# Optimization experiments

Measured on AMD Instinct MI355X. Metric: run time of the kernel, lower is better.

Reference implementation:

```python
import jax, jax.numpy as jnp
import numpy as np

BINS = 64
EPS = 1e-8


def _compute_histogram(gray, bins=BINS):
    # gray: [B, H, W] -> normalized histogram [B, bins]
    B = gray.shape[0]
    flat = gray.reshape(B, -1)                      # [B, N]
    mn = flat.min(axis=1, keepdims=True)
    mx = flat.max(axis=1, keepdims=True)
    valid = mx > mn                                  # [B, 1]
    norm = (flat - mn) / jnp.where(valid, mx - mn, 1.0)
    idx = jnp.clip((norm * (bins - 1)).astype(jnp.int32), 0, bins - 1)  # [B, N]
    # per-image bincount via scatter-add
    hist = jax.vmap(lambda i: jnp.zeros(bins, dtype=flat.dtype).at[i].add(1.0))(idx)
    hist = hist / hist.sum(axis=1, keepdims=True)
    return jnp.where(valid, hist, jnp.full_like(hist, 1.0 / bins))


def reference(x, y, lambda_cc=10.0):
    # channel balance
    x_mean = jnp.mean(x, axis=(2, 3), keepdims=True)   # [B,3,1,1]
    y_mean = jnp.mean(y, axis=(2, 3), keepdims=True)
    x_bal = x_mean / (jnp.sum(x_mean, axis=1, keepdims=True) + EPS)
    y_bal = y_mean / (jnp.sum(y_mean, axis=1, keepdims=True) + EPS)
    color_balance_loss = jnp.mean(jnp.abs(x_bal - y_bal))

    # luminance
    x_gray = 0.299 * x[:, 0] + 0.587 * x[:, 1] + 0.114 * x[:, 2]  # [B,H,W]
    y_gray = 0.299 * y[:, 0] + 0.587 * y[:, 1] + 0.114 * y[:, 2]

    x_hist = _compute_histogram(x_gray)
    y_hist = _compute_histogram(y_gray)

    # F.kl_div(log(x_hist+eps), y_hist, reduction='batchmean')
    log_in = jnp.log(x_hist + EPS)
    ylogy = jnp.where(y_hist > 0, y_hist * jnp.log(jnp.where(y_hist > 0, y_hist, 1.0)), 0.0)
    kl = jnp.sum(ylogy - y_hist * log_in) / x.shape[0]

    return lambda_cc * (color_balance_loss + kl)


def setup_inputs() -> dict:
    key = jax.random.key(0)
    k1, k2 = jax.random.split(key)
    x = jax.random.uniform(k1, (16, 3, 512, 512), dtype=jnp.float32)
    y = jax.random.uniform(k2, (16, 3, 512, 512), dtype=jnp.float32)
    return {"x": x, "y": y}
```

## Files before the change

kernel.cpp:

```cpp
#include <hip/hip_runtime.h>

#define HW_N (512 * 512)
#define BINS 64
#define BPI 64
#define TPB 256

struct ImgStats {
    double sumx[3];
    double sumy[3];
    unsigned int minx, maxx, miny, maxy;
    unsigned int histx[BINS];
    unsigned int histy[BINS];
};

__device__ __forceinline__ unsigned int f2ord(float f) {
    unsigned int u = __float_as_uint(f);
    return (u & 0x80000000u) ? ~u : (u | 0x80000000u);
}
__device__ __forceinline__ float ord2f(unsigned int u) {
    u = (u & 0x80000000u) ? (u ^ 0x80000000u) : ~u;
    return __uint_as_float(u);
}

__device__ __forceinline__ float grayf(float r, float g, float b) {
    return 0.299f * r + 0.587f * g + 0.114f * b;
}

__device__ __forceinline__ double waveSumD(double v) {
#pragma unroll
    for (int o = 32; o > 0; o >>= 1) v += __shfl_down(v, o);
    return v;
}
__device__ __forceinline__ float waveMinF(float v) {
#pragma unroll
    for (int o = 32; o > 0; o >>= 1) v = fminf(v, __shfl_down(v, o));
    return v;
}
__device__ __forceinline__ float waveMaxF(float v) {
#pragma unroll
    for (int o = 32; o > 0; o >>= 1) v = fmaxf(v, __shfl_down(v, o));
    return v;
}

__global__ void k_init(ImgStats* st, int B) {
    const int nwords = B * (int)(sizeof(ImgStats) / 4);
    unsigned int* w = (unsigned int*)st;
    for (int i = threadIdx.x; i < nwords; i += blockDim.x) w[i] = 0u;
    __syncthreads();
    for (int i = threadIdx.x; i < B * 2; i += blockDim.x) {
        int b = i >> 1;
        if (i & 1) st[b].miny = 0xFFFFFFFFu;
        else       st[b].minx = 0xFFFFFFFFu;
    }
}

__global__ __launch_bounds__(TPB) void k_reduce_gray(const float* __restrict__ x,
                                                     const float* __restrict__ y,
                                                     ImgStats* __restrict__ st,
                                                     float4* __restrict__ gx,
                                                     float4* __restrict__ gy) {
    const int b   = blockIdx.x / BPI;
    const int sub = blockIdx.x % BPI;
    const int qPerBlock = (HW_N / 4) / BPI;
    const int q0 = sub * qPerBlock;
    const size_t base = (size_t)b * 3 * HW_N;
    const size_t gbase = (size_t)b * (HW_N / 4);

    const float4* xr = (const float4*)(x + base);
    const float4* xg = (const float4*)(x + base + HW_N);
    const float4* xb = (const float4*)(x + base + 2 * HW_N);
    const float4* yr = (const float4*)(y + base);
    const float4* yg = (const float4*)(y + base + HW_N);
    const float4* yb = (const float4*)(y + base + 2 * HW_N);

    float s0 = 0.f, s1 = 0.f, s2 = 0.f;
    float t0 = 0.f, t1 = 0.f, t2 = 0.f;
    float mnx = 3.4e38f, mxx = -3.4e38f;
    float mny = 3.4e38f, mxy = -3.4e38f;

    for (int i = threadIdx.x; i < qPerBlock; i += TPB) {
        const int q = q0 + i;
        float4 r = xr[q], g = xg[q], bl = xb[q];
        s0 += (r.x + r.y) + (r.z + r.w);
        s1 += (g.x + g.y) + (g.z + g.w);
        s2 += (bl.x + bl.y) + (bl.z + bl.w);
        {
            float4 gv = make_float4(grayf(r.x, g.x, bl.x), grayf(r.y, g.y, bl.y),
                                    grayf(r.z, g.z, bl.z), grayf(r.w, g.w, bl.w));
            gx[gbase + q] = gv;
            mnx = fminf(mnx, fminf(fminf(gv.x, gv.y), fminf(gv.z, gv.w)));
            mxx = fmaxf(mxx, fmaxf(fmaxf(gv.x, gv.y), fmaxf(gv.z, gv.w)));
        }
        r = yr[q]; g = yg[q]; bl = yb[q];
        t0 += (r.x + r.y) + (r.z + r.w);
        t1 += (g.x + g.y) + (g.z + g.w);
        t2 += (bl.x + bl.y) + (bl.z + bl.w);
        {
            float4 gv = make_float4(grayf(r.x, g.x, bl.x), grayf(r.y, g.y, bl.y),
                                    grayf(r.z, g.z, bl.z), grayf(r.w, g.w, bl.w));
            gy[gbase + q] = gv;
            mny = fminf(mny, fminf(fminf(gv.x, gv.y), fminf(gv.z, gv.w)));
            mxy = fmaxf(mxy, fmaxf(fmaxf(gv.x, gv.y), fmaxf(gv.z, gv.w)));
        }
    }

    const int wave = threadIdx.x >> 6;
    const int lane = threadIdx.x & 63;
    __shared__ double shs[6][TPB / 64];
    __shared__ float  shmn[2][TPB / 64];
    __shared__ float  shmx[2][TPB / 64];

    double d;
    d = waveSumD((double)s0); if (!lane) shs[0][wave] = d;
    d = waveSumD((double)s1); if (!lane) shs[1][wave] = d;
    d = waveSumD((double)s2); if (!lane) shs[2][wave] = d;
    d = waveSumD((double)t0); if (!lane) shs[3][wave] = d;
    d = waveSumD((double)t1); if (!lane) shs[4][wave] = d;
    d = waveSumD((double)t2); if (!lane) shs[5][wave] = d;
    float f;
    f = waveMinF(mnx); if (!lane) shmn[0][wave] = f;
    f = waveMinF(mny); if (!lane) shmn[1][wave] = f;
    f = waveMaxF(mxx); if (!lane) shmx[0][wave] = f;
    f = waveMaxF(mxy); if (!lane) shmx[1][wave] = f;
    __syncthreads();

    if (threadIdx.x == 0) {
        atomicAdd(&st[b].sumx[0], shs[0][0] + shs[0][1] + shs[0][2] + shs[0][3]);
        atomicAdd(&st[b].sumx[1], shs[1][0] + shs[1][1] + shs[1][2] + shs[1][3]);
        atomicAdd(&st[b].sumx[2], shs[2][0] + shs[2][1] + shs[2][2] + shs[2][3]);
        atomicAdd(&st[b].sumy[0], shs[3][0] + shs[3][1] + shs[3][2] + shs[3][3]);
        atomicAdd(&st[b].sumy[1], shs[4][0] + shs[4][1] + shs[4][2] + shs[4][3]);
        atomicAdd(&st[b].sumy[2], shs[5][0] + shs[5][1] + shs[5][2] + shs[5][3]);
        float a;
        a = fminf(fminf(shmn[0][0], shmn[0][1]), fminf(shmn[0][2], shmn[0][3]));
        atomicMin(&st[b].minx, f2ord(a));
        a = fminf(fminf(shmn[1][0], shmn[1][1]), fminf(shmn[1][2], shmn[1][3]));
        atomicMin(&st[b].miny, f2ord(a));
        a = fmaxf(fmaxf(shmx[0][0], shmx[0][1]), fmaxf(shmx[0][2], shmx[0][3]));
        atomicMax(&st[b].maxx, f2ord(a));
        a = fmaxf(fmaxf(shmx[1][0], shmx[1][1]), fmaxf(shmx[1][2], shmx[1][3]));
        atomicMax(&st[b].maxy, f2ord(a));
    }
}

__global__ __launch_bounds__(TPB) void k_hist_gray(const float4* __restrict__ gx,
                                                   const float4* __restrict__ gy,
                                                   ImgStats* __restrict__ st) {
    __shared__ unsigned int lh[16][BINS];
    for (int i = threadIdx.x; i < 16 * BINS; i += TPB) ((unsigned int*)lh)[i] = 0u;

    const int b   = blockIdx.x / BPI;
    const int sub = blockIdx.x % BPI;

    const float mnx = ord2f(st[b].minx), mxx = ord2f(st[b].maxx);
    const float mny = ord2f(st[b].miny), mxy = ord2f(st[b].maxy);
    const float rgx = (mxx > mnx) ? (mxx - mnx) : 1.0f;
    const float rgy = (mxy > mny) ? (mxy - mny) : 1.0f;
    __syncthreads();

    const int qPerBlock = (HW_N / 4) / BPI;
    const int q0 = sub * qPerBlock;
    const size_t gbase = (size_t)b * (HW_N / 4);

    const int wave = threadIdx.x >> 6;
    const int half = (threadIdx.x >> 5) & 1;
    unsigned int* hx = lh[wave * 2 + half];
    unsigned int* hy = lh[8 + wave * 2 + half];

    for (int i = threadIdx.x; i < qPerBlock; i += TPB) {
        const float4 gvx = gx[gbase + q0 + i];
        const float4 gvy = gy[gbase + q0 + i];
        const float vx[4] = { gvx.x, gvx.y, gvx.z, gvx.w };
        const float vy[4] = { gvy.x, gvy.y, gvy.z, gvy.w };
#pragma unroll
        for (int j = 0; j < 4; j++) {
            float t = ((vx[j] - mnx) / rgx) * 63.0f;
            int id = (int)t;
            id = id < 0 ? 0 : (id > 63 ? 63 : id);
            atomicAdd(&hx[id], 1u);
        }
#pragma unroll
        for (int j = 0; j < 4; j++) {
            float t = ((vy[j] - mny) / rgy) * 63.0f;
            int id = (int)t;
            id = id < 0 ? 0 : (id > 63 ? 63 : id);
            atomicAdd(&hy[id], 1u);
        }
    }
    __syncthreads();

    for (int i = threadIdx.x; i < 2 * BINS; i += TPB) {
        const int src = i >> 6, bin = i & 63;
        unsigned int v = 0;
#pragma unroll
        for (int k = 0; k < 8; k++) v += lh[src * 8 + k][bin];
        if (v) atomicAdd(src ? &st[b].histy[bin] : &st[b].histx[bin], v);
    }
}

__global__ __launch_bounds__(TPB) void k_hist(const float* __restrict__ x,
                                              const float* __restrict__ y,
                                              ImgStats* __restrict__ st) {
    __shared__ unsigned int lh[8][BINS];
    for (int i = threadIdx.x; i < 8 * BINS; i += TPB) ((unsigned int*)lh)[i] = 0u;

    const int b   = blockIdx.x / BPI;
    const int sub = blockIdx.x % BPI;

    const float mnx = ord2f(st[b].minx), mxx = ord2f(st[b].maxx);
    const float mny = ord2f(st[b].miny), mxy = ord2f(st[b].maxy);
    const float rgx = (mxx > mnx) ? (mxx - mnx) : 1.0f;
    const float rgy = (mxy > mny) ? (mxy - mny) : 1.0f;
    __syncthreads();

    const int qPerBlock = (HW_N / 4) / BPI;
    const int q0 = sub * qPerBlock;
    const size_t base = (size_t)b * 3 * HW_N;

    const float4* xr = (const float4*)(x + base);
    const float4* xg = (const float4*)(x + base + HW_N);
    const float4* xb = (const float4*)(x + base + 2 * HW_N);
    const float4* yr = (const float4*)(y + base);
    const float4* yg = (const float4*)(y + base + HW_N);
    const float4* yb = (const float4*)(y + base + 2 * HW_N);

    const int wave = threadIdx.x >> 6;
    unsigned int* hx = lh[wave];
    unsigned int* hy = lh[4 + wave];

    for (int i = threadIdx.x; i < qPerBlock; i += TPB) {
        const int q = q0 + i;
        float4 r = xr[q], g = xg[q], bl = xb[q];
        {
            float gv[4] = { grayf(r.x, g.x, bl.x), grayf(r.y, g.y, bl.y),
                            grayf(r.z, g.z, bl.z), grayf(r.w, g.w, bl.w) };
#pragma unroll
            for (int j = 0; j < 4; j++) {
                float t = ((gv[j] - mnx) / rgx) * 63.0f;
                int id = (int)t;
                id = id < 0 ? 0 : (id > 63 ? 63 : id);
                atomicAdd(&hx[id], 1u);
            }
        }
        r = yr[q]; g = yg[q]; bl = yb[q];
        {
            float gv[4] = { grayf(r.x, g.x, bl.x), grayf(r.y, g.y, bl.y),
                            grayf(r.z, g.z, bl.z), grayf(r.w, g.w, bl.w) };
#pragma unroll
            for (int j = 0; j < 4; j++) {
                float t = ((gv[j] - mny) / rgy) * 63.0f;
                int id = (int)t;
                id = id < 0 ? 0 : (id > 63 ? 63 : id);
                atomicAdd(&hy[id], 1u);
            }
        }
    }
    __syncthreads();

    for (int i = threadIdx.x; i < 2 * BINS; i += TPB) {
        const int src = i >> 6, bin = i & 63;
        unsigned int v = lh[src * 4 + 0][bin] + lh[src * 4 + 1][bin] +
                         lh[src * 4 + 2][bin] + lh[src * 4 + 3][bin];
        if (v) atomicAdd(src ? &st[b].histy[bin] : &st[b].histx[bin], v);
    }
}

__global__ __launch_bounds__(1024) void k_final(const ImgStats* __restrict__ st,
                                                float* __restrict__ out, int B) {
    const int tid = threadIdx.x;
    double klt = 0.0, cbt = 0.0;

    for (int t = tid; t < B * BINS; t += 1024) {
        const int b = t >> 6, bin = t & 63;
        const ImgStats& s = st[b];
        const float mnx = ord2f(s.minx), mxx = ord2f(s.maxx);
        const float mny = ord2f(s.miny), mxy = ord2f(s.maxy);
        const float invN = 1.0f / (float)HW_N;
        const float xh = (mxx > mnx) ? (float)s.histx[bin] * invN : (1.0f / BINS);
        const float yh = (mxy > mny) ? (float)s.histy[bin] * invN : (1.0f / BINS);
        const float log_in = logf(xh + 1e-8f);
        const float ylogy = (yh > 0.0f) ? yh * logf(yh) : 0.0f;
        klt += (double)ylogy - (double)yh * (double)log_in;
    }

    for (int t = tid; t < B * 3; t += 1024) {
        const int b = t / 3, c = t % 3;
        const ImgStats& s = st[b];
        const double N = (double)HW_N;
        const double xb = (s.sumx[c] / N) /
                          ((s.sumx[0] + s.sumx[1] + s.sumx[2]) / N + 1e-8);
        const double yb = (s.sumy[c] / N) /
                          ((s.sumy[0] + s.sumy[1] + s.sumy[2]) / N + 1e-8);
        cbt += fabs(xb - yb);
    }

    __shared__ double skl[16], scb[16];
    const double kw = waveSumD(klt);
    const double cw = waveSumD(cbt);
    const int wave = tid >> 6, lane = tid & 63;
    if (!lane) { skl[wave] = kw; scb[wave] = cw; }
    __syncthreads();
    if (tid == 0) {
        double K = 0.0, C = 0.0;
        for (int i = 0; i < 16; i++) { K += skl[i]; C += scb[i]; }
        const double kl = K / (double)B;
        const double cb = C / (double)(B * 3);
        out[0] = (float)(10.0 * (cb + kl));
    }
}

extern "C" void kernel_launch(void* const* d_in, const int* in_sizes, int n_in,
                              void* d_out, int out_size, void* d_ws, size_t ws_size,
                              hipStream_t stream) {
    const float* x = (const float*)d_in[0];
    const float* y = (const float*)d_in[1];
    float* out = (float*)d_out;
    const int B = in_sizes[0] / (3 * HW_N);

    ImgStats* st = (ImgStats*)d_ws;

    const size_t grayBytes = (size_t)B * HW_N * sizeof(float);
    const size_t grayOff   = 16384;
    const size_t needed    = grayOff + 2 * grayBytes;

    k_init<<<1, 256, 0, stream>>>(st, B);

    if (ws_size >= needed) {
        float4* gx = (float4*)((char*)d_ws + grayOff);
        float4* gy = (float4*)((char*)d_ws + grayOff + grayBytes);
        k_reduce_gray<<<B * BPI, TPB, 0, stream>>>(x, y, st, gx, gy);
        k_hist_gray<<<B * BPI, TPB, 0, stream>>>(gx, gy, st);
    } else {
        k_reduce_gray<<<B * BPI, TPB, 0, stream>>>(x, y, st,
            (float4*)((char*)d_ws + grayOff), (float4*)((char*)d_ws + grayOff));
        k_hist<<<B * BPI, TPB, 0, stream>>>(x, y, st);
    }

    k_final<<<1, 1024, 0, stream>>>(st, out, B);
}
```

Measured before the change: 141.4 us.

## Replace global atomics with per-block partials and drop init kernel

```diff
diff --git a/kernel.cpp b/kernel.cpp
--- a/kernel.cpp
+++ b/kernel.cpp
@@ -2,25 +2,8 @@
 
 #define HW_N (512 * 512)
 #define BINS 64
-#define BPI 64
+#define BPI 128
 #define TPB 256
-
-struct ImgStats {
-    double sumx[3];
-    double sumy[3];
-    unsigned int minx, maxx, miny, maxy;
-    unsigned int histx[BINS];
-    unsigned int histy[BINS];
-};
-
-__device__ __forceinline__ unsigned int f2ord(float f) {
-    unsigned int u = __float_as_uint(f);
-    return (u & 0x80000000u) ? ~u : (u | 0x80000000u);
-}
-__device__ __forceinline__ float ord2f(unsigned int u) {
-    u = (u & 0x80000000u) ? (u ^ 0x80000000u) : ~u;
-    return __uint_as_float(u);
-}
 
 __device__ __forceinline__ float grayf(float r, float g, float b) {
     return 0.299f * r + 0.587f * g + 0.114f * b;
@@ -42,21 +25,12 @@
     return v;
 }
 
-__global__ void k_init(ImgStats* st, int B) {
-    const int nwords = B * (int)(sizeof(ImgStats) / 4);
-    unsigned int* w = (unsigned int*)st;
-    for (int i = threadIdx.x; i < nwords; i += blockDim.x) w[i] = 0u;
-    __syncthreads();
-    for (int i = threadIdx.x; i < B * 2; i += blockDim.x) {
-        int b = i >> 1;
-        if (i & 1) st[b].miny = 0xFFFFFFFFu;
-        else       st[b].minx = 0xFFFFFFFFu;
-    }
-}
-
 __global__ __launch_bounds__(TPB) void k_reduce_gray(const float* __restrict__ x,
                                                      const float* __restrict__ y,
-                                                     ImgStats* __restrict__ st,
+                                                     double* __restrict__ psum,
+                                                     float2* __restrict__ pmin,
+                                                     float2* __restrict__ pmax,
+                                                     unsigned int* __restrict__ ghist,
                                                      float4* __restrict__ gx,
                                                      float4* __restrict__ gy) {
     const int b   = blockIdx.x / BPI;
@@ -125,44 +99,60 @@
     __syncthreads();
 
     if (threadIdx.x == 0) {
-        atomicAdd(&st[b].sumx[0], shs[0][0] + shs[0][1] + shs[0][2] + shs[0][3]);
-        atomicAdd(&st[b].sumx[1], shs[1][0] + shs[1][1] + shs[1][2] + shs[1][3]);
-        atomicAdd(&st[b].sumx[2], shs[2][0] + shs[2][1] + shs[2][2] + shs[2][3]);
-        atomicAdd(&st[b].sumy[0], shs[3][0] + shs[3][1] + shs[3][2] + shs[3][3]);
-        atomicAdd(&st[b].sumy[1], shs[4][0] + shs[4][1] + shs[4][2] + shs[4][3]);
-        atomicAdd(&st[b].sumy[2], shs[5][0] + shs[5][1] + shs[5][2] + shs[5][3]);
-        float a;
-        a = fminf(fminf(shmn[0][0], shmn[0][1]), fminf(shmn[0][2], shmn[0][3]));
-        atomicMin(&st[b].minx, f2ord(a));
-        a = fminf(fminf(shmn[1][0], shmn[1][1]), fminf(shmn[1][2], shmn[1][3]));
-        atomicMin(&st[b].miny, f2ord(a));
-        a = fmaxf(fmaxf(shmx[0][0], shmx[0][1]), fmaxf(shmx[0][2], shmx[0][3]));
-        atomicMax(&st[b].maxx, f2ord(a));
-        a = fmaxf(fmaxf(shmx[1][0], shmx[1][1]), fmaxf(shmx[1][2], shmx[1][3]));
-        atomicMax(&st[b].maxy, f2ord(a));
-    }
-}
-
-__global__ __launch_bounds__(TPB) void k_hist_gray(const float4* __restrict__ gx,
-                                                   const float4* __restrict__ gy,
-                                                   ImgStats* __restrict__ st) {
+        double* ps = psum + (size_t)blockIdx.x * 6;
+        ps[0] = shs[0][0] + shs[0][1] + shs[0][2] + shs[0][3];
+        ps[1] = shs[1][0] + shs[1][1] + shs[1][2] + shs[1][3];
+        ps[2] = shs[2][0] + shs[2][1] + shs[2][2] + shs[2][3];
+        ps[3] = shs[3][0] + shs[3][1] + shs[3][2] + shs[3][3];
+        ps[4] = shs[4][0] + shs[4][1] + shs[4][2] + shs[4][3];
+        ps[5] = shs[5][0] + shs[5][1] + shs[5][2] + shs[5][3];
+        pmin[blockIdx.x] = make_float2(
+            fminf(fminf(shmn[0][0], shmn[0][1]), fminf(shmn[0][2], shmn[0][3])),
+            fminf(fminf(shmn[1][0], shmn[1][1]), fminf(shmn[1][2], shmn[1][3])));
+        pmax[blockIdx.x] = make_float2(
+            fmaxf(fmaxf(shmx[0][0], shmx[0][1]), fmaxf(shmx[0][2], shmx[0][3])),
+            fmaxf(fmaxf(shmx[1][0], shmx[1][1]), fmaxf(shmx[1][2], shmx[1][3])));
+    }
+    if (sub == 0) {
+        for (int i = threadIdx.x; i < 2 * BINS; i += TPB)
+            ghist[b * 2 * BINS + i] = 0u;
+    }
+}
+
+__global__ __launch_bounds__(TPB) void k_hist(const float4* __restrict__ gx,
+                                              const float4* __restrict__ gy,
+                                              const float2* __restrict__ pmin,
+                                              const float2* __restrict__ pmax,
+                                              unsigned int* __restrict__ ghist) {
     __shared__ unsigned int lh[16][BINS];
-    for (int i = threadIdx.x; i < 16 * BINS; i += TPB) ((unsigned int*)lh)[i] = 0u;
+    __shared__ float sred[4];
 
     const int b   = blockIdx.x / BPI;
     const int sub = blockIdx.x % BPI;
-
-    const float mnx = ord2f(st[b].minx), mxx = ord2f(st[b].maxx);
-    const float mny = ord2f(st[b].miny), mxy = ord2f(st[b].maxy);
+    const int wave = threadIdx.x >> 6;
+    const int lane = threadIdx.x & 63;
+
+    {
+        const int s0 = b * BPI;
+        float v;
+        if (wave == 0)      v = waveMinF(fminf(pmin[s0 + lane].x, pmin[s0 + 64 + lane].x));
+        else if (wave == 1) v = waveMinF(fminf(pmin[s0 + lane].y, pmin[s0 + 64 + lane].y));
+        else if (wave == 2) v = waveMaxF(fmaxf(pmax[s0 + lane].x, pmax[s0 + 64 + lane].x));
+        else                v = waveMaxF(fmaxf(pmax[s0 + lane].y, pmax[s0 + 64 + lane].y));
+        if (!lane) sred[wave] = v;
+    }
+    for (int i = threadIdx.x; i < 16 * BINS; i += TPB) ((unsigned int*)lh)[i] = 0u;
+    __syncthreads();
+
+    const float mnx = sred[0], mny = sred[1];
+    const float mxx = sred[2], mxy = sred[3];
     const float rgx = (mxx > mnx) ? (mxx - mnx) : 1.0f;
     const float rgy = (mxy > mny) ? (mxy - mny) : 1.0f;
-    __syncthreads();
 
     const int qPerBlock = (HW_N / 4) / BPI;
     const int q0 = sub * qPerBlock;
     const size_t gbase = (size_t)b * (HW_N / 4);
 
-    const int wave = threadIdx.x >> 6;
     const int half = (threadIdx.x >> 5) & 1;
     unsigned int* hx = lh[wave * 2 + half];
     unsigned int* hy = lh[8 + wave * 2 + half];
@@ -194,24 +184,39 @@
         unsigned int v = 0;
 #pragma unroll
         for (int k = 0; k < 8; k++) v += lh[src * 8 + k][bin];
-        if (v) atomicAdd(src ? &st[b].histy[bin] : &st[b].histx[bin], v);
-    }
-}
-
-__global__ __launch_bounds__(TPB) void k_hist(const float* __restrict__ x,
-                                              const float* __restrict__ y,
-                                              ImgStats* __restrict__ st) {
-    __shared__ unsigned int lh[8][BINS];
-    for (int i = threadIdx.x; i < 8 * BINS; i += TPB) ((unsigned int*)lh)[i] = 0u;
+        if (v) atomicAdd(&ghist[(b * 2 + src) * BINS + bin], v);
+    }
+}
+
+__global__ __launch_bounds__(TPB) void k_hist_src(const float* __restrict__ x,
+                                                  const float* __restrict__ y,
+                                                  const float2* __restrict__ pmin,
+                                                  const float2* __restrict__ pmax,
+                                                  unsigned int* __restrict__ ghist) {
+    __shared__ unsigned int lh[16][BINS];
+    __shared__ float sred[4];
 
     const int b   = blockIdx.x / BPI;
     const int sub = blockIdx.x % BPI;
-
-    const float mnx = ord2f(st[b].minx), mxx = ord2f(st[b].maxx);
-    const float mny = ord2f(st[b].miny), mxy = ord2f(st[b].maxy);
+    const int wave = threadIdx.x >> 6;
+    const int lane = threadIdx.x & 63;
+
+    {
+        const int s0 = b * BPI;
+        float v;
+        if (wave == 0)      v = waveMinF(fminf(pmin[s0 + lane].x, pmin[s0 + 64 + lane].x));
+        else if (wave == 1) v = waveMinF(fminf(pmin[s0 + lane].y, pmin[s0 + 64 + lane].y));
+        else if (wave == 2) v = waveMaxF(fmaxf(pmax[s0 + lane].x, pmax[s0 + 64 + lane].x));
+        else                v = waveMaxF(fmaxf(pmax[s0 + lane].y, pmax[s0 + 64 + lane].y));
+        if (!lane) sred[wave] = v;
+    }
+    for (int i = threadIdx.x; i < 16 * BINS; i += TPB) ((unsigned int*)lh)[i] = 0u;
+    __syncthreads();
+
+    const float mnx = sred[0], mny = sred[1];
+    const float mxx = sred[2], mxy = sred[3];
     const float rgx = (mxx > mnx) ? (mxx - mnx) : 1.0f;
     const float rgy = (mxy > mny) ? (mxy - mny) : 1.0f;
-    __syncthreads();
 
     const int qPerBlock = (HW_N / 4) / BPI;
     const int q0 = sub * qPerBlock;
@@ -224,9 +229,9 @@
     const float4* yg = (const float4*)(y + base + HW_N);
     const float4* yb = (const float4*)(y + base + 2 * HW_N);
 
-    const int wave = threadIdx.x >> 6;
-    unsigned int* hx = lh[wave];
-    unsigned int* hy = lh[4 + wave];
+    const int half = (threadIdx.x >> 5) & 1;
+    unsigned int* hx = lh[wave * 2 + half];
+    unsigned int* hy = lh[8 + wave * 2 + half];
 
     for (int i = threadIdx.x; i < qPerBlock; i += TPB) {
         const int q = q0 + i;
@@ -259,38 +264,60 @@
 
     for (int i = threadIdx.x; i < 2 * BINS; i += TPB) {
         const int src = i >> 6, bin = i & 63;
-        unsigned int v = lh[src * 4 + 0][bin] + lh[src * 4 + 1][bin] +
-                         lh[src * 4 + 2][bin] + lh[src * 4 + 3][bin];
-        if (v) atomicAdd(src ? &st[b].histy[bin] : &st[b].histx[bin], v);
-    }
-}
-
-__global__ __launch_bounds__(1024) void k_final(const ImgStats* __restrict__ st,
+        unsigned int v = 0;
+#pragma unroll
+        for (int k = 0; k < 8; k++) v += lh[src * 8 + k][bin];
+        if (v) atomicAdd(&ghist[(b * 2 + src) * BINS + bin], v);
+    }
+}
+
+__global__ __launch_bounds__(1024) void k_final(const double* __restrict__ psum,
+                                                const float2* __restrict__ pmin,
+                                                const float2* __restrict__ pmax,
+                                                const unsigned int* __restrict__ ghist,
                                                 float* __restrict__ out, int B) {
     const int tid = threadIdx.x;
+    __shared__ double ssum[16][6];
+    __shared__ float  smin[16][2], smax[16][2];
+
+    if (tid < B * 6) {
+        const int img = tid / 6, c = tid % 6;
+        double s = 0.0;
+        for (int k = 0; k < BPI; k++) s += psum[(size_t)(img * BPI + k) * 6 + c];
+        ssum[img][c] = s;
+    }
+    if (tid >= 128 && tid < 128 + B * 2) {
+        const int t = tid - 128;
+        const int img = t >> 1, which = t & 1;
+        float mn = 3.4e38f, mx = -3.4e38f;
+        for (int k = 0; k < BPI; k++) {
+            const float2 a = pmin[img * BPI + k];
+            const float2 c = pmax[img * BPI + k];
+            mn = fminf(mn, which ? a.y : a.x);
+            mx = fmaxf(mx, which ? c.y : c.x);
+        }
+        smin[img][which] = mn;
+        smax[img][which] = mx;
+    }
+    __syncthreads();
+
     double klt = 0.0, cbt = 0.0;
-
     for (int t = tid; t < B * BINS; t += 1024) {
         const int b = t >> 6, bin = t & 63;
-        const ImgStats& s = st[b];
-        const float mnx = ord2f(s.minx), mxx = ord2f(s.maxx);
-        const float mny = ord2f(s.miny), mxy = ord2f(s.maxy);
+        const bool vx = smax[b][0] > smin[b][0];
+        const bool vy = smax[b][1] > smin[b][1];
         const float invN = 1.0f / (float)HW_N;
-        const float xh = (mxx > mnx) ? (float)s.histx[bin] * invN : (1.0f / BINS);
-        const float yh = (mxy > mny) ? (float)s.histy[bin] * invN : (1.0f / BINS);
+        const float xh = vx ? (float)ghist[(b * 2 + 0) * BINS + bin] * invN : (1.0f / BINS);
+        const float yh = vy ? (float)ghist[(b * 2 + 1) * BINS + bin] * invN : (1.0f / BINS);
         const float log_in = logf(xh + 1e-8f);
         const float ylogy = (yh > 0.0f) ? yh * logf(yh) : 0.0f;
         klt += (double)ylogy - (double)yh * (double)log_in;
     }
-
     for (int t = tid; t < B * 3; t += 1024) {
         const int b = t / 3, c = t % 3;
-        const ImgStats& s = st[b];
         const double N = (double)HW_N;
-        const double xb = (s.sumx[c] / N) /
-                          ((s.sumx[0] + s.sumx[1] + s.sumx[2]) / N + 1e-8);
-        const double yb = (s.sumy[c] / N) /
-                          ((s.sumy[0] + s.sumy[1] + s.sumy[2]) / N + 1e-8);
+        const double xb = (ssum[b][c] / N) / ((ssum[b][0] + ssum[b][1] + ssum[b][2]) / N + 1e-8);
+        const double yb = (ssum[b][3 + c] / N) / ((ssum[b][3] + ssum[b][4] + ssum[b][5]) / N + 1e-8);
         cbt += fabs(xb - yb);
     }
 
@@ -303,9 +330,7 @@
     if (tid == 0) {
         double K = 0.0, C = 0.0;
         for (int i = 0; i < 16; i++) { K += skl[i]; C += scb[i]; }
-        const double kl = K / (double)B;
-        const double cb = C / (double)(B * 3);
-        out[0] = (float)(10.0 * (cb + kl));
+        out[0] = (float)(10.0 * (C / (double)(B * 3) + K / (double)B));
     }
 }
 
@@ -316,25 +341,33 @@
     const float* y = (const float*)d_in[1];
     float* out = (float*)d_out;
     const int B = in_sizes[0] / (3 * HW_N);
-
-    ImgStats* st = (ImgStats*)d_ws;
-
-    const size_t grayBytes = (size_t)B * HW_N * sizeof(float);
-    const size_t grayOff   = 16384;
-    const size_t needed    = grayOff + 2 * grayBytes;
-
-    k_init<<<1, 256, 0, stream>>>(st, B);
+    const int nblk = B * BPI;
+
+    char* ws = (char*)d_ws;
+    double*       psum  = (double*)(ws);
+    float2*       pmin  = (float2*)(ws + 98304);
+    float2*       pmax  = (float2*)(ws + 114688);
+    unsigned int* ghist = (unsigned int*)(ws + 131072);
+    const size_t  grayOff   = 262144;
+    const size_t  grayBytes = (size_t)B * HW_N * sizeof(float);
+    const size_t  needed    = grayOff + 2 * grayBytes;
+    (void)nblk;
 
     if (ws_size >= needed) {
-        float4* gx = (float4*)((char*)d_ws + grayOff);
-        float4* gy = (float4*)((char*)d_ws + grayOff + grayBytes);
-        k_reduce_gray<<<B * BPI, TPB, 0, stream>>>(x, y, st, gx, gy);
-        k_hist_gray<<<B * BPI, TPB, 0, stream>>>(gx, gy, st);
+        float4* gx = (float4*)(ws + grayOff);
+        float4* gy = (float4*)(ws + grayOff + grayBytes);
+        k_reduce_gray<<<B * BPI, TPB, 0, stream>>>(x, y, psum, pmin, pmax, ghist, gx, gy);
+        k_hist<<<B * BPI, TPB, 0, stream>>>(gx, gy, pmin, pmax, ghist);
     } else {
-        k_reduce_gray<<<B * BPI, TPB, 0, stream>>>(x, y, st,
-            (float4*)((char*)d_ws + grayOff), (float4*)((char*)d_ws + grayOff));
-        k_hist<<<B * BPI, TPB, 0, stream>>>(x, y, st);
-    }
-
-    k_final<<<1, 1024, 0, stream>>>(st, out, B);
-}
+        float4* scratch = (float4*)(ws + 131072 + 8192);
+        (void)scratch;
+        static float4* dummy = nullptr;
+        (void)dummy;
+        k_reduce_gray<<<B * BPI, TPB, 0, stream>>>(x, y, psum, pmin, pmax, ghist,
+                                                   (float4*)(ws + 139264),
+                                                   (float4*)(ws + 139264));
+        k_hist_src<<<B * BPI, TPB, 0, stream>>>(x, y, pmin, pmax, ghist);
+    }
+
+    k_final<<<1, 1024, 0, stream>>>(psum, pmin, pmax, ghist, out, B);
+}
```

Result: no change. 141.5 us (+0.1%).
